# Kernel optimization log

Hardware: AMD Instinct MI355X
Metric: run time of the kernel (lower is better)

## Reference

```python
import jax, jax.numpy as jnp
import numpy as np

UNITS = 1024
IN_DIM = 1024
BATCH = 4096


def setup_inputs() -> dict:
    key = jax.random.key(0)
    ks = jax.random.split(key, 11)
    C = UNITS + IN_DIM  # concat dim
    glorot = lambda k, shp: jax.random.uniform(k, shp, jnp.float32, -1.0, 1.0) * np.sqrt(6.0 / (shp[0] + shp[1]))
    return {
        "inputs": jax.random.normal(ks[0], (BATCH, IN_DIM), jnp.float32),
        "hidden_state": jax.random.normal(ks[1], (BATCH, UNITS), jnp.float32),
        "cell_state": jax.random.normal(ks[2], (BATCH, UNITS), jnp.float32),
        "W_f": glorot(ks[3], (C, UNITS)), "b_f": jnp.ones((UNITS,), jnp.float32),  # forget bias init = ones
        "W_i": glorot(ks[4], (C, UNITS)), "b_i": jnp.zeros((UNITS,), jnp.float32),
        "W_c": glorot(ks[5], (C, UNITS)), "b_c": jnp.zeros((UNITS,), jnp.float32),
        "W_o": glorot(ks[6], (C, UNITS)), "b_o": jnp.zeros((UNITS,), jnp.float32),
    }


def reference(inputs, hidden_state, cell_state, W_f, b_f, W_i, b_i, W_c, b_c, W_o, b_o):
    # concat order matches original: (hidden_state, inputs)
    x = jnp.concatenate((hidden_state, inputs), axis=1)  # [B, U+D]
    f = jax.nn.sigmoid(x @ W_f + b_f)
    i = jax.nn.sigmoid(x @ W_i + b_i)
    c_cand = jnp.tanh(x @ W_c + b_c)
    new_cell = f * cell_state + i * c_cand
    o = jax.nn.sigmoid(x @ W_o + b_o)
    new_hidden = o * jnp.tanh(new_cell)
    return (new_hidden, new_cell)
```

## Files before the change

### kernel.cpp

```cpp
#include <hip/hip_runtime.h>
#include <hip/hip_bf16.h>

#define BATCH  4096
#define UNITS  1024
#define CDIM   2048
#define NDIM   4096

typedef __attribute__((ext_vector_type(8))) short bf16x8;
typedef __attribute__((ext_vector_type(4))) short bf16x4;
typedef __attribute__((ext_vector_type(4))) float f32x4;

__device__ __forceinline__ void gload_lds16(const void* g, void* l) {
    __builtin_amdgcn_global_load_lds(
        (const __attribute__((address_space(1))) unsigned int*)g,
        (__attribute__((address_space(3))) unsigned int*)l, 16, 0, 0);
}

__device__ __forceinline__ float sigm(float x) { return 1.f / (1.f + __expf(-x)); }
__device__ __forceinline__ float tanh_fast(float x) { return 2.f / (1.f + __expf(-2.f * x)) - 1.f; }

__device__ __forceinline__ short f2bf(float f) {
    __hip_bfloat16 h = __float2bfloat16(f);
    return *reinterpret_cast<short*>(&h);
}

__global__ __launch_bounds__(256) void prep(
        const float* __restrict__ h, const float* __restrict__ in,
        const float* __restrict__ Wf, const float* __restrict__ Wi,
        const float* __restrict__ Wc, const float* __restrict__ Wo,
        __hip_bfloat16* __restrict__ x, __hip_bfloat16* __restrict__ Wt) {
    __shared__ float lds[64 * 65];
    int b = blockIdx.x, tid = threadIdx.x;
    if (b < 4096) {
        int t   = b * 256 + tid;
        int row = t >> 8;
        int c8  = (t & 255) << 3;
        const float* src = (c8 < UNITS) ? (h + (size_t)row * UNITS + c8)
                                        : (in + (size_t)row * UNITS + (c8 - UNITS));
        float4 v0 = ((const float4*)src)[0];
        float4 v1 = ((const float4*)src)[1];
        bf16x8 o;
        o[0] = f2bf(v0.x); o[1] = f2bf(v0.y); o[2] = f2bf(v0.z); o[3] = f2bf(v0.w);
        o[4] = f2bf(v1.x); o[5] = f2bf(v1.y); o[6] = f2bf(v1.z); o[7] = f2bf(v1.w);
        *(bf16x8*)(x + (size_t)row * CDIM + c8) = o;
    } else {
        int idx = b - 4096;
        int g = idx >> 9, kt = (idx >> 4) & 31, ut = idx & 15;
        const float* W = (g == 0) ? Wf : (g == 1) ? Wi : (g == 2) ? Wc : Wo;
        int k0 = kt * 64, u0 = ut * 64;
        int r16 = tid & 15, hi = tid >> 4;
#pragma unroll
        for (int it = 0; it < 4; ++it) {
            int kl = it * 16 + hi;
            float4 v = *(const float4*)&W[(size_t)(k0 + kl) * UNITS + u0 + r16 * 4];
            float* d = &lds[kl * 65 + r16 * 4];
            d[0] = v.x; d[1] = v.y; d[2] = v.z; d[3] = v.w;
        }
        __syncthreads();
#pragma unroll
        for (int it = 0; it < 4; ++it) {
            int ul = it * 16 + hi;
            int u  = u0 + ul;
            int n  = ((u >> 5) << 7) + (((u >> 4) & 1) << 6) + (g << 4) + (u & 15);
            bf16x4 o;
#pragma unroll
            for (int j = 0; j < 4; ++j) o[j] = f2bf(lds[(r16 * 4 + j) * 65 + ul]);
            *(bf16x4*)(Wt + (size_t)n * CDIM + k0 + r16 * 4) = o;
        }
    }
}

__global__ __launch_bounds__(256, 2) void gemm_lstm(
    const __hip_bfloat16* __restrict__ A,
    const __hip_bfloat16* __restrict__ Bt,
    const float* __restrict__ b_f, const float* __restrict__ b_i,
    const float* __restrict__ b_c, const float* __restrict__ b_o,
    const float* __restrict__ cell,
    float* __restrict__ out)
{
    __shared__ short As[2][128 * 64];
    const int K = CDIM;

    int bid = blockIdx.x;
    int nb  = (bid & 7) * 2 + ((bid >> 3) & 1);
    int mb  = bid >> 4;
    int m0  = mb * 128, n0 = nb * 256;

    int tid  = threadIdx.x;
    int w    = tid >> 6, lane = tid & 63;
    int quad = lane >> 4, r16 = lane & 15;
    int wn   = w * 64;

    f32x4 acc[8][4];
#pragma unroll
    for (int i = 0; i < 8; ++i)
#pragma unroll
        for (int j = 0; j < 4; ++j) acc[i][j] = (f32x4){0.f, 0.f, 0.f, 0.f};

    const short* Ag = (const short*)A  + (size_t)m0 * K;
    const short* Bg = (const short*)Bt + (size_t)(n0 + wn + r16) * K + quad * 8;

    auto stageA = [&](int p, int k0) {
#pragma unroll
        for (int q = 0; q < 4; ++q) {
            int s    = q * 256 + tid;
            int row  = s >> 3;
            int cg   = (s & 7) ^ (row & 7);
            int lofs = (q * 256 + w * 64) * 8;
            gload_lds16(Ag + (size_t)row * K + k0 + cg * 8, &As[p][lofs]);
        }
    };

    bf16x8 bcur[8], bnxt[8];
#pragma unroll
    for (int ks = 0; ks < 2; ++ks)
#pragma unroll
        for (int j = 0; j < 4; ++j)
            bcur[ks * 4 + j] = *(const bf16x8*)&Bg[(size_t)(j * 16) * K + ks * 32];
    stageA(0, 0);

    for (int kt = 0; kt < K / 64; ++kt) {
        int p = kt & 1;
        asm volatile("s_waitcnt vmcnt(0)" ::: "memory");
        __syncthreads();
        if (kt + 1 < K / 64) {
            stageA(1 - p, (kt + 1) * 64);
            int kb = (kt + 1) * 64;
#pragma unroll
            for (int ks = 0; ks < 2; ++ks)
#pragma unroll
                for (int j = 0; j < 4; ++j)
                    bnxt[ks * 4 + j] = *(const bf16x8*)&Bg[(size_t)(j * 16) * K + kb + ks * 32];
        }
#pragma unroll
        for (int ks = 0; ks < 2; ++ks) {
            bf16x8 af[8];
            int kc = ((quad + ks * 4) ^ (r16 & 7)) * 8;
#pragma unroll
            for (int i = 0; i < 8; ++i)
                af[i] = *(const bf16x8*)&As[p][(i * 16 + r16) * 64 + kc];
#pragma unroll
            for (int i = 0; i < 8; ++i)
#pragma unroll
                for (int j = 0; j < 4; ++j)
                    acc[i][j] = __builtin_amdgcn_mfma_f32_16x16x32_bf16(af[i], bcur[ks * 4 + j], acc[i][j], 0, 0, 0);
        }
#pragma unroll
        for (int t = 0; t < 8; ++t) bcur[t] = bnxt[t];
    }

    int u = nb * 64 + (w >> 1) * 32 + (w & 1) * 16 + r16;
    float bfv = b_f[u], biv = b_i[u], bcv = b_c[u], bov = b_o[u];
    float* out_h = out;
    float* out_c = out + (size_t)BATCH * UNITS;
#pragma unroll
    for (int i = 0; i < 8; ++i) {
#pragma unroll
        for (int rr = 0; rr < 4; ++rr) {
            int m = m0 + i * 16 + quad * 4 + rr;
            float fg = sigm(acc[i][0][rr] + bfv);
            float ig = sigm(acc[i][1][rr] + biv);
            float cc = tanh_fast(acc[i][2][rr] + bcv);
            float og = sigm(acc[i][3][rr] + bov);
            float cold = cell[(size_t)m * UNITS + u];
            float cn = fg * cold + ig * cc;
            out_h[(size_t)m * UNITS + u] = og * tanh_fast(cn);
            out_c[(size_t)m * UNITS + u] = cn;
        }
    }
}

extern "C" void kernel_launch(void* const* d_in, const int* in_sizes, int n_in,
                              void* d_out, int out_size, void* d_ws, size_t ws_size,
                              hipStream_t stream) {
    const float* inputs = (const float*)d_in[0];
    const float* hidden = (const float*)d_in[1];
    const float* cell   = (const float*)d_in[2];
    const float* Wf = (const float*)d_in[3];
    const float* bf_ = (const float*)d_in[4];
    const float* Wi = (const float*)d_in[5];
    const float* bi_ = (const float*)d_in[6];
    const float* Wc = (const float*)d_in[7];
    const float* bc_ = (const float*)d_in[8];
    const float* Wo = (const float*)d_in[9];
    const float* bo_ = (const float*)d_in[10];
    float* out = (float*)d_out;

    char* ws = (char*)d_ws;
    __hip_bfloat16* x  = (__hip_bfloat16*)ws;
    __hip_bfloat16* Wt = (__hip_bfloat16*)(ws + (16u << 20));

    prep<<<dim3(6144), dim3(256), 0, stream>>>(hidden, inputs, Wf, Wi, Wc, Wo, x, Wt);
    gemm_lstm<<<dim3(512), dim3(256), 0, stream>>>(
        x, Wt, bf_, bi_, bc_, bo_, cell, out);
}
```

Measured before the change: 219.3 us.

## Stage B tiles through LDS with triple-buffered K=32 pipeline

Result: faster. 211.8 us (-3.4%).

```diff
diff --git a/kernel.cpp b/kernel.cpp
--- a/kernel.cpp
+++ b/kernel.cpp
@@ -78,8 +78,10 @@
     const float* __restrict__ cell,
     float* __restrict__ out)
 {
-    __shared__ short As[2][128 * 64];
+    __shared__ alignas(16) short As[3][128 * 32];
+    __shared__ alignas(16) short Bs[3][256 * 32];
     const int K = CDIM;
+    const int NT = K / 32;
 
     int bid = blockIdx.x;
     int nb  = (bid & 7) * 2 + ((bid >> 3) & 1);
@@ -98,55 +100,54 @@
         for (int j = 0; j < 4; ++j) acc[i][j] = (f32x4){0.f, 0.f, 0.f, 0.f};
 
     const short* Ag = (const short*)A  + (size_t)m0 * K;
-    const short* Bg = (const short*)Bt + (size_t)(n0 + wn + r16) * K + quad * 8;
+    const short* Bg = (const short*)Bt + (size_t)n0 * K;
 
-    auto stageA = [&](int p, int k0) {
+    auto stage = [&](short* Al, short* Bl, int kt) {
+        int k0 = kt * 32;
+#pragma unroll
+        for (int q = 0; q < 2; ++q) {
+            int s = q * 256 + tid;
+            int row = s >> 2, c = (s & 3) ^ (row & 3);
+            gload_lds16(Ag + (size_t)row * K + k0 + c * 8, Al + (q * 256 + wn) * 8);
+        }
 #pragma unroll
         for (int q = 0; q < 4; ++q) {
-            int s    = q * 256 + tid;
-            int row  = s >> 3;
-            int cg   = (s & 7) ^ (row & 7);
-            int lofs = (q * 256 + w * 64) * 8;
-            gload_lds16(Ag + (size_t)row * K + k0 + cg * 8, &As[p][lofs]);
+            int s = q * 256 + tid;
+            int n = s >> 2, c = (s & 3) ^ (n & 3);
+            gload_lds16(Bg + (size_t)n * K + k0 + c * 8, Bl + (q * 256 + wn) * 8);
         }
     };
 
-    bf16x8 bcur[8], bnxt[8];
+    short *a0 = &As[0][0], *a1 = &As[1][0], *a2 = &As[2][0];
+    short *b0 = &Bs[0][0], *b1 = &Bs[1][0], *b2 = &Bs[2][0];
+    stage(a0, b0, 0);
+    stage(a1, b1, 1);
+
+    for (int t = 0; t < NT; ++t) {
+        if (t < NT - 1) asm volatile("s_waitcnt vmcnt(6)" ::: "memory");
+        else            asm volatile("s_waitcnt vmcnt(0)" ::: "memory");
+        __builtin_amdgcn_s_barrier();
+        if (t + 2 < NT) stage(a2, b2, t + 2);
+
+        int kc = (quad ^ (r16 & 3)) * 8;
+        bf16x8 af[8], bf[4];
 #pragma unroll
-    for (int ks = 0; ks < 2; ++ks)
+        for (int i = 0; i < 8; ++i)
+            af[i] = *(const bf16x8*)&a0[(i * 16 + r16) * 32 + kc];
 #pragma unroll
         for (int j = 0; j < 4; ++j)
-            bcur[ks * 4 + j] = *(const bf16x8*)&Bg[(size_t)(j * 16) * K + ks * 32];
-    stageA(0, 0);
+            bf[j] = *(const bf16x8*)&b0[(wn + j * 16 + r16) * 32 + kc];
 
-    for (int kt = 0; kt < K / 64; ++kt) {
-        int p = kt & 1;
-        asm volatile("s_waitcnt vmcnt(0)" ::: "memory");
-        __syncthreads();
-        if (kt + 1 < K / 64) {
-            stageA(1 - p, (kt + 1) * 64);
-            int kb = (kt + 1) * 64;
+        __builtin_amdgcn_s_setprio(1);
 #pragma unroll
-            for (int ks = 0; ks < 2; ++ks)
+        for (int i = 0; i < 8; ++i)
 #pragma unroll
-                for (int j = 0; j < 4; ++j)
-                    bnxt[ks * 4 + j] = *(const bf16x8*)&Bg[(size_t)(j * 16) * K + kb + ks * 32];
-        }
-#pragma unroll
-        for (int ks = 0; ks < 2; ++ks) {
-            bf16x8 af[8];
-            int kc = ((quad + ks * 4) ^ (r16 & 7)) * 8;
-#pragma unroll
-            for (int i = 0; i < 8; ++i)
-                af[i] = *(const bf16x8*)&As[p][(i * 16 + r16) * 64 + kc];
-#pragma unroll
-            for (int i = 0; i < 8; ++i)
-#pragma unroll
-                for (int j = 0; j < 4; ++j)
-                    acc[i][j] = __builtin_amdgcn_mfma_f32_16x16x32_bf16(af[i], bcur[ks * 4 + j], acc[i][j], 0, 0, 0);
-        }
-#pragma unroll
-        for (int t = 0; t < 8; ++t) bcur[t] = bnxt[t];
+            for (int j = 0; j < 4; ++j)
+                acc[i][j] = __builtin_amdgcn_mfma_f32_16x16x32_bf16(af[i], bf[j], acc[i][j], 0, 0, 0);
+        __builtin_amdgcn_s_setprio(0);
+
+        short* ta = a0; a0 = a1; a1 = a2; a2 = ta;
+        short* tb = b0; b0 = b1; b1 = b2; b2 = tb;
     }
 
     int u = nb * 64 + (w >> 1) * 32 + (w & 1) * 16 + r16;
```

## Triple-buffer A tiles with two-ahead prefetch and partial vmcnt waits

Applied to the files above, without the earlier changes.

Measured after the change: 222.9 us. About the same (+1.6%).

```diff
diff --git a/kernel.cpp b/kernel.cpp
--- a/kernel.cpp
+++ b/kernel.cpp
@@ -78,7 +78,9 @@
     const float* __restrict__ cell,
     float* __restrict__ out)
 {
-    __shared__ short As[2][128 * 64];
+    __shared__ alignas(16) short As0[128 * 64];
+    __shared__ alignas(16) short As1[128 * 64];
+    __shared__ alignas(16) short As2[128 * 64];
     const int K = CDIM;
 
     int bid = blockIdx.x;
@@ -100,54 +102,71 @@
     const short* Ag = (const short*)A  + (size_t)m0 * K;
     const short* Bg = (const short*)Bt + (size_t)(n0 + wn + r16) * K + quad * 8;
 
-    auto stageA = [&](int p, int k0) {
-#pragma unroll
-        for (int q = 0; q < 4; ++q) {
-            int s    = q * 256 + tid;
-            int row  = s >> 3;
-            int cg   = (s & 7) ^ (row & 7);
-            int lofs = (q * 256 + w * 64) * 8;
-            gload_lds16(Ag + (size_t)row * K + k0 + cg * 8, &As[p][lofs]);
-        }
-    };
-
     bf16x8 bcur[8], bnxt[8];
+
+#define STAGEA(DST, KT)                                                        \
+    { int k0_ = (KT) * 64;                                                     \
+      _Pragma("unroll")                                                        \
+      for (int q = 0; q < 4; ++q) {                                            \
+          int s_ = q * 256 + tid, row_ = s_ >> 3, cg_ = (s_ & 7) ^ (row_ & 7); \
+          gload_lds16(Ag + (size_t)row_ * K + k0_ + cg_ * 8,                   \
+                      DST + (q * 256 + w * 64) * 8);                           \
+      } }
+
+#define KSTEP(T, CUR, NXT2, DOB, DOS, WN)                                      \
+    {                                                                          \
+        asm volatile("s_waitcnt vmcnt(" #WN ")" ::: "memory");                 \
+        __builtin_amdgcn_s_barrier();                                          \
+        if (DOB) {                                                             \
+            int kb_ = ((T) + 1) * 64;                                          \
+            _Pragma("unroll")                                                  \
+            for (int ks = 0; ks < 2; ++ks)                                     \
+                _Pragma("unroll")                                              \
+                for (int j = 0; j < 4; ++j)                                    \
+                    bnxt[ks * 4 + j] =                                         \
+                        *(const bf16x8*)&Bg[(size_t)(j * 16) * K + kb_ + ks * 32]; \
+        }                                                                      \
+        if (DOS) STAGEA(NXT2, (T) + 2);                                        \
+        _Pragma("unroll")                                                      \
+        for (int ks = 0; ks < 2; ++ks) {                                       \
+            bf16x8 af[8];                                                      \
+            int kc_ = ((quad + ks * 4) ^ (r16 & 7)) * 8;                       \
+            _Pragma("unroll")                                                  \
+            for (int i = 0; i < 8; ++i)                                        \
+                af[i] = *(const bf16x8*)&CUR[(i * 16 + r16) * 64 + kc_];       \
+            __builtin_amdgcn_s_setprio(1);                                     \
+            _Pragma("unroll")                                                  \
+            for (int i = 0; i < 8; ++i)                                        \
+                _Pragma("unroll")                                              \
+                for (int j = 0; j < 4; ++j)                                    \
+                    acc[i][j] = __builtin_amdgcn_mfma_f32_16x16x32_bf16(       \
+                        af[i], bcur[ks * 4 + j], acc[i][j], 0, 0, 0);          \
+            __builtin_amdgcn_s_setprio(0);                                     \
+        }                                                                      \
+        if (DOB) {                                                             \
+            _Pragma("unroll")                                                  \
+            for (int tt = 0; tt < 8; ++tt) bcur[tt] = bnxt[tt];                \
+        }                                                                      \
+    }
+
+    STAGEA(As0, 0);
 #pragma unroll
     for (int ks = 0; ks < 2; ++ks)
 #pragma unroll
         for (int j = 0; j < 4; ++j)
             bcur[ks * 4 + j] = *(const bf16x8*)&Bg[(size_t)(j * 16) * K + ks * 32];
-    stageA(0, 0);
-
-    for (int kt = 0; kt < K / 64; ++kt) {
-        int p = kt & 1;
-        asm volatile("s_waitcnt vmcnt(0)" ::: "memory");
-        __syncthreads();
-        if (kt + 1 < K / 64) {
-            stageA(1 - p, (kt + 1) * 64);
-            int kb = (kt + 1) * 64;
-#pragma unroll
-            for (int ks = 0; ks < 2; ++ks)
-#pragma unroll
-                for (int j = 0; j < 4; ++j)
-                    bnxt[ks * 4 + j] = *(const bf16x8*)&Bg[(size_t)(j * 16) * K + kb + ks * 32];
-        }
-#pragma unroll
-        for (int ks = 0; ks < 2; ++ks) {
-            bf16x8 af[8];
-            int kc = ((quad + ks * 4) ^ (r16 & 7)) * 8;
-#pragma unroll
-            for (int i = 0; i < 8; ++i)
-                af[i] = *(const bf16x8*)&As[p][(i * 16 + r16) * 64 + kc];
-#pragma unroll
-            for (int i = 0; i < 8; ++i)
-#pragma unroll
-                for (int j = 0; j < 4; ++j)
-                    acc[i][j] = __builtin_amdgcn_mfma_f32_16x16x32_bf16(af[i], bcur[ks * 4 + j], acc[i][j], 0, 0, 0);
-        }
-#pragma unroll
-        for (int t = 0; t < 8; ++t) bcur[t] = bnxt[t];
-    }
+    STAGEA(As1, 1);
+
+    for (int t0 = 0; t0 < 30; t0 += 3) {
+        KSTEP(t0,     As0, As2, true, true, 4)
+        KSTEP(t0 + 1, As1, As0, true, true, 4)
+        KSTEP(t0 + 2, As2, As1, true, true, 4)
+    }
+    KSTEP(30, As0, As2, true,  false, 4)
+    KSTEP(31, As1, As0, false, false, 0)
+
+#undef KSTEP
+#undef STAGEA
 
     int u = nb * 64 + (w >> 1) * 32 + (w & 1) * 16 + r16;
     float bfv = b_f[u], biv = b_i[u], bcv = b_c[u], bov = b_o[u];
```
